# Performance work log

Hardware: AMD Instinct MI355X
Metric: run time of the kernel (lower is better)

Reference implementation:

```python
import jax, jax.numpy as jnp
import numpy as np

EPS = 1e-5

def _conv1x1(x, w, b):
    # x: [B,C,H,W], w: [O,C,1,1], b: [O]
    return jnp.einsum('oc,bchw->bohw', w[:, :, 0, 0], x) + b[None, :, None, None]

def _maxpool(x, s):
    return jax.lax.reduce_window(x, -jnp.inf, jax.lax.max,
                                 (1, 1, s, s), (1, 1, s, s), 'VALID')

def _sra(x, gw, gb, tw, tb, pw, pb, ww, wb, scale):
    # embedded-Gaussian non-local block with spatial sub-sampling on phi/g
    B, C, H, W = x.shape
    ic = gw.shape[0]
    g = _maxpool(_conv1x1(x, gw, gb), scale).reshape(B, ic, -1)    # [B,ic,n]
    phi = _maxpool(_conv1x1(x, pw, pb), scale).reshape(B, ic, -1)  # [B,ic,n]
    theta = _conv1x1(x, tw, tb).reshape(B, ic, -1)                 # [B,ic,N]
    f = jnp.einsum('bcn,bcm->bnm', theta, phi)                     # [B,N,n]
    a = jax.nn.softmax(f, axis=-1)
    y = jnp.einsum('bnm,bcm->bcn', a, g).reshape(B, ic, H, W)
    return _conv1x1(y, ww, wb) + x

def _conv_bn(x, w, gamma, beta, mean, var):
    y = jax.lax.conv_general_dilated(x, w, (1, 1), ((1, 1), (1, 1)),
                                     dimension_numbers=('NCHW', 'OIHW', 'NCHW'))
    inv = gamma / jnp.sqrt(var + EPS)
    return y * inv[None, :, None, None] + (beta - mean * inv)[None, :, None, None]

def setup_inputs() -> dict:
    key = jax.random.key(0)
    B, C = 4, 32
    sizes = [96, 48, 24]
    inp = {}
    ks = iter(jax.random.split(key, 64))
    for i, hw in enumerate(sizes):
        inp[f'fea1_{i}'] = jax.random.normal(next(ks), (B, C, hw, hw), jnp.float32)
        inp[f'fea2_{i}'] = jax.random.normal(next(ks), (B, C, hw, hw), jnp.float32)
    for lv in (1, 2, 3):
        for nm in ('g', 't', 'p'):
            inp[f'{nm}{lv}_w'] = jax.random.normal(next(ks), (C, 2 * C, 1, 1), jnp.float32) * 0.05
            inp[f'{nm}{lv}_b'] = jax.random.normal(next(ks), (C,), jnp.float32) * 0.05
        inp[f'w{lv}_w'] = jax.random.normal(next(ks), (2 * C, C, 1, 1), jnp.float32) * 0.05
        inp[f'w{lv}_b'] = jax.random.normal(next(ks), (2 * C,), jnp.float32) * 0.05
        inp[f'c{lv}_w'] = jax.random.normal(next(ks), (C, 2 * C, 3, 3), jnp.float32) * 0.05
        inp[f'bn{lv}_g'] = jax.random.uniform(next(ks), (C,), jnp.float32, 0.5, 1.5)
        inp[f'bn{lv}_b'] = jax.random.normal(next(ks), (C,), jnp.float32) * 0.05
        inp[f'bn{lv}_m'] = jax.random.normal(next(ks), (C,), jnp.float32) * 0.05
        inp[f'bn{lv}_v'] = jax.random.uniform(next(ks), (C,), jnp.float32, 0.5, 1.5)
    return inp

def reference(fea1_0, fea1_1, fea1_2, fea2_0, fea2_1, fea2_2,
              g1_w, g1_b, t1_w, t1_b, p1_w, p1_b, w1_w, w1_b, c1_w, bn1_g, bn1_b, bn1_m, bn1_v,
              g2_w, g2_b, t2_w, t2_b, p2_w, p2_b, w2_w, w2_b, c2_w, bn2_g, bn2_b, bn2_m, bn2_v,
              g3_w, g3_b, t3_w, t3_b, p3_w, p3_b, w3_w, w3_b, c3_w, bn3_g, bn3_b, bn3_m, bn3_v):
    x1 = jnp.concatenate([fea1_0, fea2_0], axis=1)
    x2 = jnp.concatenate([fea1_1, fea2_1], axis=1)
    x3 = jnp.concatenate([fea1_2, fea2_2], axis=1)
    z1 = _sra(x1, g1_w, g1_b, t1_w, t1_b, p1_w, p1_b, w1_w, w1_b, 2)
    z2 = _sra(x2, g2_w, g2_b, t2_w, t2_b, p2_w, p2_b, w2_w, w2_b, 4)
    z3 = _sra(x3, g3_w, g3_b, t3_w, t3_b, p3_w, p3_b, w3_w, w3_b, 8)
    out1 = _conv_bn(z1, c1_w, bn1_g, bn1_b, bn1_m, bn1_v)
    out2 = _conv_bn(z2, c2_w, bn2_g, bn2_b, bn2_m, bn2_v)
    out3 = _conv_bn(z3, c3_w, bn3_g, bn3_b, bn3_m, bn3_v)
    return (out1, out2, out3)
```

## Files before the change

### kernel.cpp

```cpp
#include <hip/hip_runtime.h>
#include <hip/hip_bf16.h>

typedef __hip_bfloat16 bf16;
typedef __attribute__((ext_vector_type(8))) short short8;
typedef __attribute__((ext_vector_type(4))) float floatx4;

__device__ __forceinline__ float b2f(bf16 v) { return __bfloat162float(v); }
__device__ __forceinline__ bf16 f2b(float v) { return __float2bfloat16(v); }
__device__ __forceinline__ float ldv(const void* p, size_t i, bool f32) {
    return f32 ? ((const float*)p)[i] : b2f(((const bf16*)p)[i]);
}
template <bool F32>
__device__ __forceinline__ float ldt(const void* p, size_t i) {
    return F32 ? ((const float*)p)[i] : b2f(((const bf16*)p)[i]);
}
__device__ __forceinline__ float s2f(short s) {
    unsigned int u = ((unsigned int)(unsigned short)s) << 16;
    float f; __builtin_memcpy(&f, &u, 4); return f;
}
__device__ __forceinline__ short f2s(float f) {
    bf16 h = f2b(f); short s; __builtin_memcpy(&s, &h, 2); return s;
}
__device__ __forceinline__ bool uflag(const int* flag) {
    return __builtin_amdgcn_readfirstlane(flag[0]) != 0;
}
#define MFMA16(a, b, c) __builtin_amdgcn_mfma_f32_16x16x32_bf16(a, b, c, 0, 0, 0)

struct Ptrs { const void* p[45]; };

struct Lvl {
    const void *f1, *f2;
    const float *btgp, *wbf, *bfold;
    const bf16 *Wb, *Wt, *Wc3;
    bf16 *th, *g, *p, *phi, *gt, *yp, *z;
    float* lp;
    int N, n, npad, nch, W, s, wp, H, tX, BN;
    size_t outOff;
};

#define O_BTGP  0
#define O_WBF   96
#define O_BFOLD 160
#define O_WT    192
#define O_WC3   1216
#define O_WB    10432
#define LVS     13504

__global__ void k_prep(Ptrs in, int* flag, float* __restrict__ wsf)
{
    __shared__ int scnt;
    if (threadIdx.x == 0) scnt = 0;
    __syncthreads();
    {
        const unsigned short* us = (const unsigned short*)in.p[0];
        int local = 0;
        for (int i = threadIdx.x; i < 8192; i += 256) {
            unsigned e = us[2 * i] & 0x7F80u;
            if (e == 0x7F80u || e == 0u) local++;
        }
        atomicAdd(&scnt, local);
    }
    __syncthreads();
    bool f32 = scnt >= 8;
    if (blockIdx.x == 0 && blockIdx.y == 0 && threadIdx.x == 0) flag[0] = f32 ? 1 : 0;

    int lv = blockIdx.y;
    float* base = wsf + (size_t)lv * LVS;
    const int wb0 = 6 + 13 * lv;
    const void* gw  = in.p[wb0 + 0];
    const void* gb  = in.p[wb0 + 1];
    const void* tw  = in.p[wb0 + 2];
    const void* tb  = in.p[wb0 + 3];
    const void* pw  = in.p[wb0 + 4];
    const void* pb  = in.p[wb0 + 5];
    const void* ww  = in.p[wb0 + 6];
    const void* wb  = in.p[wb0 + 7];
    const void* cw  = in.p[wb0 + 8];
    const void* bng = in.p[wb0 + 9];
    const void* bnb = in.p[wb0 + 10];
    const void* bnm = in.p[wb0 + 11];
    const void* bnv = in.p[wb0 + 12];
    int gid = blockIdx.x * 256 + threadIdx.x;
    int stride = gridDim.x * 256;

    float* btgp = base + O_BTGP;
    float* wbf = base + O_WBF;
    float* bfold = base + O_BFOLD;
    bf16* Wt = (bf16*)(base + O_WT);
    bf16* Wc3 = (bf16*)(base + O_WC3);
    bf16* Wb = (bf16*)(base + O_WB);

    for (int e = gid; e < 96 * 64; e += stride) {
        int o = e >> 6, k = e & 63;
        float v;
        if (o < 32)      v = ldv(tw, (size_t)o * 64 + k, f32);
        else if (o < 64) v = ldv(gw, (size_t)(o - 32) * 64 + k, f32);
        else             v = ldv(pw, (size_t)(o - 64) * 64 + k, f32);
        Wb[e] = f2b(v);
    }
    for (int e = gid; e < 96; e += stride) {
        float v = (e < 32) ? ldv(tb, e, f32)
                           : (e < 64 ? ldv(gb, e - 32, f32) : ldv(pb, e - 64, f32));
        btgp[e] = v;
    }
    for (int e = gid; e < 64 * 32; e += stride)
        Wt[e] = f2b(ldv(ww, e, f32));
    for (int e = gid; e < 64; e += stride) wbf[e] = ldv(wb, e, f32);
    for (int e = gid; e < 18432; e += stride) {
        int k = e & 31, n = (e >> 5) & 15, ot = (e >> 9) & 1;
        int tap = (e >> 10) % 9, cc = e / 9216;
        int o = ot * 16 + n, c = cc * 32 + k;
        float inv = ldv(bng, o, f32) * rsqrtf(ldv(bnv, o, f32) + 1e-5f);
        Wc3[e] = f2b(ldv(cw, ((size_t)o * 64 + c) * 9 + tap, f32) * inv);
    }
    for (int e = gid; e < 32; e += stride) {
        float inv = ldv(bng, e, f32) * rsqrtf(ldv(bnv, e, f32) + 1e-5f);
        bfold[e] = ldv(bnb, e, f32) - ldv(bnm, e, f32) * inv;
    }
}

template <bool F32>
__device__ __forceinline__ void tgpm_body(const Lvl& P, int rb)
{
    __shared__ __align__(16) bf16 X[64 * 72];
    int tid = threadIdx.x, lane = tid & 63, wv = tid >> 6;
    int quad = lane >> 4, col = lane & 15;
    int row0 = rb * 64;
    int b = row0 / P.N;
    int pix0 = row0 - b * P.N;

#pragma unroll
    for (int it = 0; it < 16; it++) {
        int e = it * 256 + tid;
        int pix = e & 63, c = e >> 6;
        const void* fx = (c < 32) ? P.f1 : P.f2;
        int cc = c & 31;
        float v = ldt<F32>(fx, (size_t)(b * 32 + cc) * P.N + pix0 + pix);
        X[pix * 72 + c] = f2b(v);
    }
    __syncthreads();

    short8 a_lo = *(const short8*)(X + (wv * 16 + col) * 72 + quad * 8);
    short8 a_hi = *(const short8*)(X + (wv * 16 + col) * 72 + 32 + quad * 8);
    const floatx4 zc = {0.f, 0.f, 0.f, 0.f};
#pragma unroll
    for (int ot = 0; ot < 6; ot++) {
        const bf16* wp = P.Wb + (size_t)(ot * 16 + col) * 64 + quad * 8;
        short8 b_lo = *(const short8*)(wp);
        short8 b_hi = *(const short8*)(wp + 32);
        floatx4 acc = MFMA16(a_lo, b_lo, zc);
        acc = MFMA16(a_hi, b_hi, acc);
        float bias = P.btgp[ot * 16 + col];
        bf16* dst = (ot < 2) ? P.th : ((ot < 4) ? P.g : P.p);
        int och = (ot & 1) * 16 + col;
#pragma unroll
        for (int r = 0; r < 4; r++) {
            int pix = row0 + wv * 16 + quad * 4 + r;
            dst[(size_t)pix * 32 + och] = f2b(acc[r] + bias);
        }
    }
}

__global__ void k_tgpm(Lvl a0, Lvl a1, Lvl a2, int s1, int s2, const int* flag)
{
    int bid = blockIdx.x;
    const Lvl P = bid < s1 ? a0 : (bid < s2 ? a1 : a2);
    int rb = bid - (bid < s1 ? 0 : (bid < s2 ? s1 : s2));
    if (uflag(flag)) tgpm_body<true>(P, rb);
    else             tgpm_body<false>(P, rb);
}

__global__ void k_pool(Lvl a0, Lvl a1, Lvl a2, int s1, int s2)
{
    int bid = blockIdx.x;
    const Lvl P = bid < s1 ? a0 : (bid < s2 ? a1 : a2);
    int local = bid - (bid < s1 ? 0 : (bid < s2 ? s1 : s2));
    int gid = local * 256 + threadIdx.x;
    int npad = P.npad;
    if (gid >= 4 * npad * 32) return;
    int c = gid & 31;
    int j = (gid >> 5) % npad;
    int b = gid / (32 * npad);
    float mg = 0.f, mp = 0.f;
    if (j < P.n) {
        int py = j / P.wp, px = j - py * P.wp;
        const int N = P.N;
        mg = -INFINITY; mp = -INFINITY;
        for (int dy = 0; dy < P.s; dy++)
            for (int dx = 0; dx < P.s; dx++) {
                int idx = (py * P.s + dy) * P.W + px * P.s + dx;
                size_t bse = ((size_t)b * N + idx) * 32 + c;
                mg = fmaxf(mg, b2f(P.g[bse]));
                mp = fmaxf(mp, b2f(P.p[bse]));
            }
    }
    P.phi[((size_t)b * npad + j) * 32 + c] = f2b(mp);
    P.gt[((size_t)b * 32 + c) * npad + j] = f2b(mg);
}

__launch_bounds__(256)
__global__ void k_attn(Lvl a0, Lvl a1, Lvl a2, int s1, int s2)
{
    __shared__ __align__(16) bf16 Pt_s[4 * 1152];
    int bid = blockIdx.x;
    const Lvl P = bid < s1 ? a0 : (bid < s2 ? a1 : a2);
    int local = bid - (bid < s1 ? 0 : (bid < s2 ? s1 : s2));
    int rowblocks = P.BN >> 6;
    int c = local / rowblocks;
    int rb = local - c * rowblocks;

    int tid = threadIdx.x, lane = tid & 63, wv = tid >> 6;
    int quad = lane >> 4, col = lane & 15;
    bf16* Pt = Pt_s + wv * 1152;
    int row0 = rb * 64;
    int b = row0 / P.N;
    int npad = P.npad;

    int T = npad >> 6, C = P.nch;
    int js = ((T * c) / C) << 6;
    int je = ((T * (c + 1)) / C) << 6;

    short8 ta = *(const short8*)(P.th + (size_t)(row0 + wv * 16 + col) * 32 + quad * 8);
    const bf16* php = P.phi + (size_t)b * npad * 32 + (size_t)col * 32 + quad * 8;
    const bf16* gtp = P.gt + (size_t)b * 32 * npad + (size_t)col * npad + quad * 8;

    floatx4 y0 = {0.f, 0.f, 0.f, 0.f}, y1 = {0.f, 0.f, 0.f, 0.f};
    float lp4[4] = {0.f, 0.f, 0.f, 0.f};
    const floatx4 zc = {0.f, 0.f, 0.f, 0.f};

    for (int j0 = js; j0 < je; j0 += 64) {
        floatx4 s0 = MFMA16(ta, *(const short8*)(php + (size_t)(j0 +  0) * 32), zc);
        floatx4 s1 = MFMA16(ta, *(const short8*)(php + (size_t)(j0 + 16) * 32), zc);
        floatx4 s2 = MFMA16(ta, *(const short8*)(php + (size_t)(j0 + 32) * 32), zc);
        floatx4 s3 = MFMA16(ta, *(const short8*)(php + (size_t)(j0 + 48) * 32), zc);
#pragma unroll
        for (int r = 0; r < 4; r++) {
            float p0 = __expf(s0[r]), p1 = __expf(s1[r]);
            float p2 = __expf(s2[r]), p3 = __expf(s3[r]);
            lp4[r] += (p0 + p1) + (p2 + p3);
            bf16* pr = Pt + (quad * 4 + r) * 72;
            pr[ 0 + col] = f2b(p0);
            pr[16 + col] = f2b(p1);
            pr[32 + col] = f2b(p2);
            pr[48 + col] = f2b(p3);
        }
#pragma unroll
        for (int kc = 0; kc < 2; kc++) {
            short8 pa = *(const short8*)(Pt + col * 72 + kc * 32 + quad * 8);
            short8 g0 = *(const short8*)(gtp + j0 + kc * 32);
            short8 g1 = *(const short8*)(gtp + (size_t)16 * npad + j0 + kc * 32);
            y0 = MFMA16(pa, g0, y0);
            y1 = MFMA16(pa, g1, y1);
        }
    }

#pragma unroll
    for (int r = 0; r < 4; r++) {
        float v = lp4[r];
        v += __shfl_xor(v, 1); v += __shfl_xor(v, 2);
        v += __shfl_xor(v, 4); v += __shfl_xor(v, 8);
        int grow = row0 + wv * 16 + quad * 4 + r;
        size_t o = ((size_t)c * P.BN + grow) * 32;
        P.yp[o + col] = f2b(y0[r]);
        P.yp[o + 16 + col] = f2b(y1[r]);
        if (col == 0) P.lp[(size_t)c * P.BN + grow] = v;
    }
}

__launch_bounds__(256)
__global__ void k_merge(Lvl a0, Lvl a1, Lvl a2, int s1, int s2, const int* flag)
{
    bool f32 = uflag(flag);
    __shared__ __align__(16) float zb[64 * 65];
    int bid = blockIdx.x;
    const Lvl P = bid < s1 ? a0 : (bid < s2 ? a1 : a2);
    int rb = bid - (bid < s1 ? 0 : (bid < s2 ? s1 : s2));
    int tid = threadIdx.x, lane = tid & 63, wv = tid >> 6;
    int quad = lane >> 4, col = lane & 15;
    int row0 = rb * 64;
    int b = row0 / P.N;
    int pix0 = row0 - b * P.N;

    int grow = row0 + wv * 16 + col;
    float yv[8] = {0.f, 0.f, 0.f, 0.f, 0.f, 0.f, 0.f, 0.f};
    float L = -(float)(P.npad - P.n);
    for (int cc = 0; cc < P.nch; cc++) {
        short8 v = *(const short8*)(P.yp + ((size_t)cc * P.BN + grow) * 32 + quad * 8);
#pragma unroll
        for (int j = 0; j < 8; j++) yv[j] += s2f(v[j]);
        L += P.lp[(size_t)cc * P.BN + grow];
    }
    float invL = 1.f / L;
    short8 ya;
#pragma unroll
    for (int j = 0; j < 8; j++) ya[j] = f2s(yv[j] * invL);

    const floatx4 zc = {0.f, 0.f, 0.f, 0.f};
    floatx4 zt[4];
#pragma unroll
    for (int ot = 0; ot < 4; ot++) {
        short8 wbv = *(const short8*)(P.Wt + (size_t)(ot * 16 + col) * 32 + quad * 8);
        zt[ot] = MFMA16(ya, wbv, zc);
    }
#pragma unroll
    for (int ot = 0; ot < 4; ot++)
#pragma unroll
        for (int r = 0; r < 4; r++)
            zb[(wv * 16 + quad * 4 + r) * 65 + ot * 16 + col] = zt[ot][r];
    __syncthreads();

    const void* fx = (wv < 2) ? P.f1 : P.f2;
    if (f32) {
#pragma unroll
        for (int k = 0; k < 16; k++) {
            int o = wv * 16 + k, op = o & 31;
            float a = zb[lane * 65 + o] + P.wbf[o];
            a += ((const float*)fx)[(size_t)(b * 32 + op) * P.N + pix0 + lane];
            P.z[((size_t)(b * 64 + o)) * P.N + pix0 + lane] = f2b(a);
        }
    } else {
#pragma unroll
        for (int k = 0; k < 16; k++) {
            int o = wv * 16 + k, op = o & 31;
            float a = zb[lane * 65 + o] + P.wbf[o];
            a += b2f(((const bf16*)fx)[(size_t)(b * 32 + op) * P.N + pix0 + lane]);
            P.z[((size_t)(b * 64 + o)) * P.N + pix0 + lane] = f2b(a);
        }
    }
}

__launch_bounds__(512)
__global__ void k_conv3m(Lvl a0, Lvl a1, Lvl a2, int s1, int s2,
                         void* out, const int* flag)
{
    bool f32 = uflag(flag);
    __shared__ __align__(16) char smem[44064];
    bf16* zh = (bf16*)smem;
    float* facc = (float*)smem;
    int bid = blockIdx.x;
    const Lvl P = bid < s1 ? a0 : (bid < s2 ? a1 : a2);
    int local = bid - (bid < s1 ? 0 : (bid < s2 ? s1 : s2));
    const int H = P.H, W = H, Npix = H * W, tX = P.tX;
    int tid = threadIdx.x, lane = tid & 63, wv = tid >> 6;
    int cc = wv >> 2, wv4 = wv & 3;
    int quad = lane >> 4, col = lane & 15;
    int tpi = tX * tX;
    int b = local / tpi;
    int t = local - b * tpi;
    int ty = t / tX, tx = t - ty * tX;
    int y0 = ty * 16, x0 = tx * 16;

    for (int e = tid; e < 2 * 324 * 32; e += 512) {
        int ch = e / 324, pix = e - ch * 324;
        int hy = pix / 18, hx = pix - hy * 18;
        int gy = y0 - 1 + hy, gx = x0 - 1 + hx;
        bf16 v = f2b(0.f);
        if (gy >= 0 && gy < H && gx >= 0 && gx < W)
            v = P.z[((size_t)(b * 64 + ch)) * Npix + gy * W + gx];
        zh[(ch >> 5) * 11016 + pix * 34 + (ch & 31)] = v;
    }
    __syncthreads();

    short8 Bf[9][2];
    const bf16* wp = P.Wc3 + (size_t)cc * 9216 + col * 32 + quad * 8;
#pragma unroll
    for (int tap = 0; tap < 9; tap++)
#pragma unroll
        for (int ot = 0; ot < 2; ot++)
            Bf[tap][ot] = *(const short8*)(wp + (tap * 2 + ot) * 512);

    floatx4 acc[4][2];
#pragma unroll
    for (int pt = 0; pt < 4; pt++)
#pragma unroll
        for (int ot = 0; ot < 2; ot++) acc[pt][ot] = (floatx4){0.f, 0.f, 0.f, 0.f};

    const bf16* zbp = zh + cc * 11016;
#pragma unroll
    for (int pt = 0; pt < 4; pt++) {
        int yy = wv4 * 4 + pt;
#pragma unroll
        for (int tap = 0; tap < 9; tap++) {
            int dy = tap / 3, dx = tap - dy * 3;
            short8 A = *(const short8*)(zbp + ((yy + dy) * 18 + (col + dx)) * 34 + quad * 8);
            acc[pt][0] = MFMA16(A, Bf[tap][0], acc[pt][0]);
            acc[pt][1] = MFMA16(A, Bf[tap][1], acc[pt][1]);
        }
    }
    __syncthreads();

    if (cc == 1) {
#pragma unroll
        for (int pt = 0; pt < 4; pt++)
#pragma unroll
            for (int ot = 0; ot < 2; ot++)
#pragma unroll
                for (int r = 0; r < 4; r++)
                    facc[((wv4 * 4 + pt) * 16 + quad * 4 + r) * 33 + ot * 16 + col]
                        = acc[pt][ot][r];
    }
    __syncthreads();

    if (cc == 0) {
#pragma unroll
        for (int pt = 0; pt < 4; pt++) {
            int oy = y0 + wv4 * 4 + pt;
            if (oy >= H) continue;
#pragma unroll
            for (int ot = 0; ot < 2; ot++) {
                int o = ot * 16 + col;
                size_t ob = P.outOff + (size_t)(b * 32 + o) * Npix + (size_t)oy * W;
                float bias = P.bfold[o];
#pragma unroll
                for (int r = 0; r < 4; r++) {
                    int ox = x0 + quad * 4 + r;
                    if (ox >= W) continue;
                    float a = acc[pt][ot][r] + bias
                            + facc[((wv4 * 4 + pt) * 16 + quad * 4 + r) * 33 + o];
                    if (f32) ((float*)out)[ob + ox] = a;
                    else     ((bf16*)out)[ob + ox] = f2b(a);
                }
            }
        }
    }
}

extern "C" void kernel_launch(void* const* d_in, const int* in_sizes, int n_in,
                              void* d_out, int out_size, void* d_ws, size_t ws_size,
                              hipStream_t stream)
{
    const int Hs[3] = {96, 48, 24};
    const int ss[3] = {2, 4, 8};
    const int npads[3] = {2304, 192, 64};
    const size_t outOff[3] = {0, 1179648, 1474560};
    const int BNs[3] = {36864, 9216, 2304};

    int nch[3] = {2, 2, 1};

    int* flag = (int*)d_ws;
    float* wsf = (float*)d_ws + 16;
    float* lpbase = wsf + 3 * LVS;
    size_t lpo[3], lpacc = 0;
    for (int lv = 0; lv < 3; lv++) { lpo[lv] = lpacc; lpacc += (size_t)nch[lv] * BNs[lv]; }
    bf16* bb = (bf16*)(lpbase + lpacc);

    const size_t gpo[3] = {0, 2359296, 2949120};
    size_t ypo[3], ypacc = 0;
    for (int lv = 0; lv < 3; lv++) { ypo[lv] = ypacc; ypacc += (size_t)nch[lv] * BNs[lv] * 32; }
    size_t Asz = ypacc > 3096576 ? ypacc : 3096576;
    const size_t tho[3] = {0, 1179648, 1474560};
    const size_t pho[3] = {1548288, 2138112, 2187264};
    const size_t gto[3] = {1843200, 2162688, 2195456};
    const size_t zo[3]  = {0, 2359296, 2949120};

    Ptrs hp;
    for (int i = 0; i < 45 && i < n_in; i++) hp.p[i] = d_in[i];
    k_prep<<<dim3(8, 3), 256, 0, stream>>>(hp, flag, wsf);

    Lvl L[3];
    for (int lv = 0; lv < 3; lv++) {
        int H = Hs[lv], N = H * H;
        float* base = wsf + (size_t)lv * LVS;
        L[lv].f1 = d_in[2 * lv];
        L[lv].f2 = d_in[2 * lv + 1];
        L[lv].btgp = base + O_BTGP;
        L[lv].wbf = base + O_WBF;
        L[lv].bfold = base + O_BFOLD;
        L[lv].Wt = (const bf16*)(base + O_WT);
        L[lv].Wc3 = (const bf16*)(base + O_WC3);
        L[lv].Wb = (const bf16*)(base + O_WB);
        L[lv].g = bb + gpo[lv];
        L[lv].p = bb + gpo[lv] + (size_t)4 * N * 32;
        L[lv].yp = bb + ypo[lv];
        L[lv].th = bb + Asz + tho[lv];
        L[lv].phi = bb + Asz + pho[lv];
        L[lv].gt = bb + Asz + gto[lv];
        L[lv].z = bb + Asz + zo[lv];
        L[lv].lp = lpbase + lpo[lv];
        L[lv].N = N;
        L[lv].n = (H / ss[lv]) * (H / ss[lv]);
        L[lv].npad = npads[lv];
        L[lv].nch = nch[lv];
        L[lv].W = H;
        L[lv].s = ss[lv];
        L[lv].wp = H / ss[lv];
        L[lv].H = H;
        L[lv].tX = (H + 15) / 16;
        L[lv].BN = 4 * N;
        L[lv].outOff = outOff[lv];
    }

    int a0 = nch[0] * (BNs[0] >> 6), a1 = nch[1] * (BNs[1] >> 6), a2 = nch[2] * (BNs[2] >> 6);
    k_tgpm<<<756, 256, 0, stream>>>(L[0], L[1], L[2], 576, 720, flag);
    k_pool<<<1280, 256, 0, stream>>>(L[0], L[1], L[2], 1152, 1248);
    k_attn<<<a0 + a1 + a2, 256, 0, stream>>>(L[0], L[1], L[2], a0, a0 + a1);
    k_merge<<<756, 256, 0, stream>>>(L[0], L[1], L[2], 576, 720, flag);
    k_conv3m<<<196, 512, 0, stream>>>(L[0], L[1], L[2], 144, 180, d_out, flag);
}
```

Baseline: 291.7 us.

## Stage phi/g tiles in double-buffered LDS and fold log2e into theta

The attention kernel now loads each 64-wide phi and g tile cooperatively into shared memory with double buffering, prefetching the next tile into registers while the current one is consumed. All four waves share one copy instead of each issuing redundant global loads. Theta weights and bias are pre-scaled by log2(e) so the softmax numerator can use exp2f directly. This adds a block-wide barrier per tile iteration and more LDS use per block, which may reduce occupancy.

```diff
diff --git a/kernel.cpp b/kernel.cpp
--- a/kernel.cpp
+++ b/kernel.cpp
@@ -82,6 +82,7 @@
     const void* bnv = in.p[wb0 + 12];
     int gid = blockIdx.x * 256 + threadIdx.x;
     int stride = gridDim.x * 256;
+    const float LOG2E = 1.44269504088896f;
 
     float* btgp = base + O_BTGP;
     float* wbf = base + O_WBF;
@@ -93,13 +94,13 @@
     for (int e = gid; e < 96 * 64; e += stride) {
         int o = e >> 6, k = e & 63;
         float v;
-        if (o < 32)      v = ldv(tw, (size_t)o * 64 + k, f32);
+        if (o < 32)      v = ldv(tw, (size_t)o * 64 + k, f32) * LOG2E;
         else if (o < 64) v = ldv(gw, (size_t)(o - 32) * 64 + k, f32);
         else             v = ldv(pw, (size_t)(o - 64) * 64 + k, f32);
         Wb[e] = f2b(v);
     }
     for (int e = gid; e < 96; e += stride) {
-        float v = (e < 32) ? ldv(tb, e, f32)
+        float v = (e < 32) ? ldv(tb, e, f32) * LOG2E
                            : (e < 64 ? ldv(gb, e - 32, f32) : ldv(pb, e - 64, f32));
         btgp[e] = v;
     }
@@ -201,7 +202,7 @@
 __launch_bounds__(256)
 __global__ void k_attn(Lvl a0, Lvl a1, Lvl a2, int s1, int s2)
 {
-    __shared__ __align__(16) bf16 Pt_s[4 * 1152];
+    __shared__ __align__(16) bf16 smem[14336];
     int bid = blockIdx.x;
     const Lvl P = bid < s1 ? a0 : (bid < s2 ? a1 : a2);
     int local = bid - (bid < s1 ? 0 : (bid < s2 ? s1 : s2));
@@ -211,7 +212,7 @@
 
     int tid = threadIdx.x, lane = tid & 63, wv = tid >> 6;
     int quad = lane >> 4, col = lane & 15;
-    bf16* Pt = Pt_s + wv * 1152;
+    bf16* Pt = smem + 9728 + wv * 1152;
     int row0 = rb * 64;
     int b = row0 / P.N;
     int npad = P.npad;
@@ -221,22 +222,43 @@
     int je = ((T * (c + 1)) / C) << 6;
 
     short8 ta = *(const short8*)(P.th + (size_t)(row0 + wv * 16 + col) * 32 + quad * 8);
-    const bf16* php = P.phi + (size_t)b * npad * 32 + (size_t)col * 32 + quad * 8;
-    const bf16* gtp = P.gt + (size_t)b * 32 * npad + (size_t)col * npad + quad * 8;
+
+    const bf16* phsrc = P.phi + ((size_t)b * npad + (tid >> 2)) * 32 + (tid & 3) * 8;
+    const bf16* gsrc  = P.gt + ((size_t)b * 32 + (tid >> 3)) * npad + (tid & 7) * 8;
+    int phdst = (tid >> 2) * 40 + (tid & 3) * 8;
+    int gdst  = 2560 + (tid >> 3) * 72 + (tid & 7) * 8;
+
+    {
+        short8 pv = *(const short8*)(phsrc + (size_t)js * 32);
+        short8 gv = *(const short8*)(gsrc + js);
+        *(short8*)(smem + phdst) = pv;
+        *(short8*)(smem + gdst) = gv;
+    }
+    __syncthreads();
 
     floatx4 y0 = {0.f, 0.f, 0.f, 0.f}, y1 = {0.f, 0.f, 0.f, 0.f};
     float lp4[4] = {0.f, 0.f, 0.f, 0.f};
     const floatx4 zc = {0.f, 0.f, 0.f, 0.f};
 
+    int cur = 0;
     for (int j0 = js; j0 < je; j0 += 64) {
-        floatx4 s0 = MFMA16(ta, *(const short8*)(php + (size_t)(j0 +  0) * 32), zc);
-        floatx4 s1 = MFMA16(ta, *(const short8*)(php + (size_t)(j0 + 16) * 32), zc);
-        floatx4 s2 = MFMA16(ta, *(const short8*)(php + (size_t)(j0 + 32) * 32), zc);
-        floatx4 s3 = MFMA16(ta, *(const short8*)(php + (size_t)(j0 + 48) * 32), zc);
+        bool hasN = (j0 + 64) < je;
+        short8 phN, ggN;
+        if (hasN) {
+            phN = *(const short8*)(phsrc + (size_t)(j0 + 64) * 32);
+            ggN = *(const short8*)(gsrc + j0 + 64);
+        }
+        const bf16* pbuf = smem + cur * 4864;
+        const bf16* gbuf = pbuf + 2560;
+
+        floatx4 s0 = MFMA16(ta, *(const short8*)(pbuf + (col) * 40 + quad * 8), zc);
+        floatx4 s1 = MFMA16(ta, *(const short8*)(pbuf + (16 + col) * 40 + quad * 8), zc);
+        floatx4 s2 = MFMA16(ta, *(const short8*)(pbuf + (32 + col) * 40 + quad * 8), zc);
+        floatx4 s3 = MFMA16(ta, *(const short8*)(pbuf + (48 + col) * 40 + quad * 8), zc);
 #pragma unroll
         for (int r = 0; r < 4; r++) {
-            float p0 = __expf(s0[r]), p1 = __expf(s1[r]);
-            float p2 = __expf(s2[r]), p3 = __expf(s3[r]);
+            float p0 = exp2f(s0[r]), p1 = exp2f(s1[r]);
+            float p2 = exp2f(s2[r]), p3 = exp2f(s3[r]);
             lp4[r] += (p0 + p1) + (p2 + p3);
             bf16* pr = Pt + (quad * 4 + r) * 72;
             pr[ 0 + col] = f2b(p0);
@@ -247,11 +269,17 @@
 #pragma unroll
         for (int kc = 0; kc < 2; kc++) {
             short8 pa = *(const short8*)(Pt + col * 72 + kc * 32 + quad * 8);
-            short8 g0 = *(const short8*)(gtp + j0 + kc * 32);
-            short8 g1 = *(const short8*)(gtp + (size_t)16 * npad + j0 + kc * 32);
+            short8 g0 = *(const short8*)(gbuf + col * 72 + kc * 32 + quad * 8);
+            short8 g1 = *(const short8*)(gbuf + (16 + col) * 72 + kc * 32 + quad * 8);
             y0 = MFMA16(pa, g0, y0);
             y1 = MFMA16(pa, g1, y1);
         }
+        if (hasN) {
+            *(short8*)(smem + (cur ^ 1) * 4864 + phdst) = phN;
+            *(short8*)(smem + (cur ^ 1) * 4864 + gdst) = ggN;
+        }
+        __syncthreads();
+        cur ^= 1;
     }
 
 #pragma unroll
```

New measurement: 265.3 us. 9.0% less time.
